# Kernel optimization log

Measured on AMD Instinct MI355X. Metric: run time of the kernel, lower is better.

Reference implementation:

```python
import jax, jax.numpy as jnp
import numpy as np

MASK_WEIGHT = 1.0
HEAD_DIM = 64
SCALING = HEAD_DIM ** -0.5


def _rotate_half(x):
    x1, x2 = jnp.split(x, 2, axis=-1)
    return jnp.concatenate([-x2, x1], axis=-1)


def _rope_tables(seq_len, dim, dtype):
    inv_freq = 1.0 / (10000.0 ** (jnp.arange(0, dim, 2, dtype=jnp.float32) / dim))
    t = jnp.arange(seq_len, dtype=jnp.float32)
    freqs = jnp.outer(t, inv_freq)                      # (s, d/2)
    cos = jnp.tile(jnp.cos(freqs), (1, 2)).astype(dtype)  # (s, d)  '(2 d)' tiling
    sin = jnp.tile(jnp.sin(freqs), (1, 2)).astype(dtype)
    return cos, sin


def _apply_rope(x, cos, sin):
    # x: (b, h, s, d); cos/sin: (s, d) broadcast over b, h
    return x * cos + _rotate_half(x) * sin


def setup_inputs() -> dict:
    key = jax.random.key(0)
    ks = jax.random.split(key, 6)
    b, h, s, d = 2, 16, 2048, 64
    d_model = h * d
    return {
        "q": jax.random.normal(ks[0], (b, h, s, d), jnp.float32),
        "k": jax.random.normal(ks[1], (b, h, s, d), jnp.float32),
        "v": jax.random.normal(ks[2], (b, h, s, d), jnp.float32),
        "attention_mask": jax.random.normal(ks[3], (1, h, s, s), jnp.float32) * 0.05,
        "out_w": jax.random.normal(ks[4], (d_model, d_model), jnp.float32) * (d_model ** -0.5),
        "out_b": jax.random.normal(ks[5], (d_model,), jnp.float32) * 0.02,
    }


def reference(q, k, v, attention_mask, out_w, out_b):
    b, h, s, d = q.shape
    cos, sin = _rope_tables(s, d, q.dtype)
    qr = _apply_rope(q, cos, sin)
    kr = _apply_rope(k, cos, sin)
    # learned per-head affinity transform of the queries: q' = (mask_weight * W) @ q
    W = attention_mask[0] * MASK_WEIGHT                    # (h, s, s), shared over batch
    qt = jnp.einsum('hqk,bhkd->bhqd', W, qr)
    # flash-style online softmax over keys == plain stable softmax (same math)
    scores = jnp.einsum('bhqd,bhkd->bhqk', qt, kr) * SCALING
    attn = jax.nn.softmax(scores, axis=-1)
    ctx = jnp.einsum('bhqk,bhkd->bhqd', attn, v)
    ctx = ctx.transpose(0, 2, 1, 3).reshape(b, s, h * d)   # (b, s, d_model)
    return ctx @ out_w.T + out_b
```

## Files before the change

### kernel.cpp

```cpp
#include <hip/hip_runtime.h>
#include <hip/hip_bf16.h>
#include <math.h>

typedef __bf16 bf16_t;
typedef __bf16 bf16x4 __attribute__((ext_vector_type(4)));
typedef __bf16 bf16x8 __attribute__((ext_vector_type(8)));
typedef float f32x4 __attribute__((ext_vector_type(4)));

#define NB 2
#define NH 16
#define SEQ 2048
#define HD 64
#define DMODEL 1024
#define QK_SCALE 0.125f
#define LOG2E 1.44269504088896340f
#define INV_2PI 0.15915494309189535f

__device__ __forceinline__ bf16_t to_bf16(float x) { return (bf16_t)x; }
#define MFMA16 __builtin_amdgcn_mfma_f32_16x16x32_bf16

__global__ __launch_bounds__(256) void k1_rope_pack(
    const float* __restrict__ q, const float* __restrict__ k, const float* __restrict__ v,
    bf16_t* __restrict__ qrT, bf16_t* __restrict__ krN, bf16_t* __restrict__ vT)
{
  __shared__ bf16_t tile[64][65];
  const int tid = threadIdx.x;
  const int blk = blockIdx.x;
  const int st = blk & 31;
  const int bh = blk >> 5;
  const int s0 = st * 64;

  const size_t base_sd = ((size_t)bh * SEQ + s0) * HD;
  const float* qb = q + base_sd;
  const float* kb = k + base_sd;
  const float* vb = v + base_sd;
  bf16_t* qrTb = qrT + (size_t)bh * HD * SEQ;
  bf16_t* krNb = krN + base_sd;
  bf16_t* vTb  = vT  + (size_t)bh * HD * SEQ;

  #pragma unroll
  for (int pp = 0; pp < 8; ++pp) {
    int idx = pp * 256 + tid;
    int sr = idx >> 5;
    int j  = idx & 31;
    float freq = __builtin_amdgcn_exp2f(-(float)j * (13.287712379549449f / 32.0f));
    float ang = (float)(s0 + sr) * freq;
    float rev = ang * INV_2PI;
    rev = rev - floorf(rev);
    float c  = __builtin_amdgcn_cosf(rev);
    float sn = __builtin_amdgcn_sinf(rev);
    float q1 = qb[sr*HD + j], q2 = qb[sr*HD + j + 32];
    tile[sr][j]      = to_bf16((q1*c - q2*sn) * QK_SCALE);
    tile[sr][j + 32] = to_bf16((q2*c + q1*sn) * QK_SCALE);
    float ka = kb[sr*HD + j], kbv = kb[sr*HD + j + 32];
    krNb[sr*HD + j]      = to_bf16(ka*c - kbv*sn);
    krNb[sr*HD + j + 32] = to_bf16(kbv*c + ka*sn);
  }
  __syncthreads();
  #pragma unroll
  for (int c = 0; c < 2; ++c) {
    int id = c*256 + tid;
    int d = id >> 3;
    int sc = (id & 7) * 8;
    bf16x8 vec;
    #pragma unroll
    for (int i = 0; i < 8; ++i) vec[i] = tile[sc + i][d];
    *(bf16x8*)&qrTb[(size_t)d * SEQ + s0 + sc] = vec;
  }
  __syncthreads();
  #pragma unroll
  for (int c = 0; c < 4; ++c) {
    int id = c*256 + tid;
    int sr = id >> 4;
    int c4 = (id & 15) * 4;
    float4 v4 = *(const float4*)&vb[sr*HD + c4];
    tile[sr][c4+0] = to_bf16(v4.x);
    tile[sr][c4+1] = to_bf16(v4.y);
    tile[sr][c4+2] = to_bf16(v4.z);
    tile[sr][c4+3] = to_bf16(v4.w);
  }
  __syncthreads();
  #pragma unroll
  for (int c = 0; c < 2; ++c) {
    int id = c*256 + tid;
    int d = id >> 3;
    int sc = (id & 7) * 8;
    bf16x8 vec;
    #pragma unroll
    for (int i = 0; i < 8; ++i) vec[i] = tile[sc + i][d];
    *(bf16x8*)&vTb[(size_t)d * SEQ + s0 + sc] = vec;
  }
}

__global__ __launch_bounds__(256) void k2_qt_gemm(
    const float* __restrict__ Wm,
    const bf16_t* __restrict__ qrT,
    bf16_t* __restrict__ qtT)
{
  __shared__ __align__(16) bf16_t A_lds[2][64*72];
  __shared__ __align__(16) bf16_t B_lds[64*72];
  const int tid = threadIdx.x;
  const int blk = blockIdx.x;
  const int n0 = (blk & 31) * 64;
  const int h = blk >> 5;
  const int wave = tid >> 6, lane = tid & 63;
  const int l15 = lane & 15, quad = lane >> 4;
  const int rs = tid >> 2, cs = (tid & 3) * 16;

  const float* Wh = Wm + (size_t)h * SEQ * SEQ + (size_t)n0 * SEQ;
  const bf16_t* A0 = qrT + ((size_t)h * HD + rs) * SEQ;
  const bf16_t* A1 = qrT + (((size_t)NH + h) * HD + rs) * SEQ;

  f32x4 acc[2][4] = {};
  float4 wreg[4];
  bf16x8 areg[2][2];

  #pragma unroll
  for (int i = 0; i < 4; ++i) wreg[i] = *(const float4*)&Wh[(size_t)rs*SEQ + cs + i*4];
  #pragma unroll
  for (int i = 0; i < 2; ++i) {
    areg[0][i] = *(const bf16x8*)&A0[cs + i*8];
    areg[1][i] = *(const bf16x8*)&A1[cs + i*8];
  }

  for (int it = 0; it < SEQ/64; ++it) {
    if (it) __syncthreads();
    #pragma unroll
    for (int i = 0; i < 2; ++i) {
      *(bf16x8*)&A_lds[0][rs*72 + cs + i*8] = areg[0][i];
      *(bf16x8*)&A_lds[1][rs*72 + cs + i*8] = areg[1][i];
      bf16x8 wb;
      float4 wa = wreg[i*2], wc = wreg[i*2+1];
      wb[0]=to_bf16(wa.x); wb[1]=to_bf16(wa.y); wb[2]=to_bf16(wa.z); wb[3]=to_bf16(wa.w);
      wb[4]=to_bf16(wc.x); wb[5]=to_bf16(wc.y); wb[6]=to_bf16(wc.z); wb[7]=to_bf16(wc.w);
      *(bf16x8*)&B_lds[rs*72 + cs + i*8] = wb;
    }
    __syncthreads();
    if (it + 1 < SEQ/64) {
      int kb = (it + 1) * 64;
      #pragma unroll
      for (int i = 0; i < 4; ++i) wreg[i] = *(const float4*)&Wh[(size_t)rs*SEQ + kb + cs + i*4];
      #pragma unroll
      for (int i = 0; i < 2; ++i) {
        areg[0][i] = *(const bf16x8*)&A0[kb + cs + i*8];
        areg[1][i] = *(const bf16x8*)&A1[kb + cs + i*8];
      }
    }
    #pragma unroll
    for (int kc = 0; kc < 2; ++kc) {
      const int off = kc*32 + quad*8;
      bf16x8 bfr[4];
      #pragma unroll
      for (int nt = 0; nt < 4; ++nt)
        bfr[nt] = *(const bf16x8*)&B_lds[(nt*16 + l15)*72 + off];
      #pragma unroll
      for (int b2 = 0; b2 < 2; ++b2) {
        bf16x8 af = *(const bf16x8*)&A_lds[b2][(wave*16 + l15)*72 + off];
        #pragma unroll
        for (int nt = 0; nt < 4; ++nt)
          acc[b2][nt] = MFMA16(af, bfr[nt], acc[b2][nt], 0, 0, 0);
      }
    }
  }
  #pragma unroll
  for (int b2 = 0; b2 < 2; ++b2)
    #pragma unroll
    for (int nt = 0; nt < 4; ++nt)
      #pragma unroll
      for (int r = 0; r < 4; ++r) {
        int d = wave*16 + quad*4 + r;
        qtT[(((size_t)b2*NH + h)*HD + d)*SEQ + n0 + nt*16 + l15] =
            to_bf16(acc[b2][nt][r] * LOG2E);
      }
}

__global__ __launch_bounds__(256, 2) void k3_flash(
    const bf16_t* __restrict__ qtT,
    const bf16_t* __restrict__ krN,
    const bf16_t* __restrict__ vT,
    bf16_t* __restrict__ ctx)
{
  __shared__ __align__(16) bf16_t K_lds[64*72];
  __shared__ __align__(16) bf16_t V_lds[64*72];
  __shared__ __align__(16) bf16_t P_lds[4][16*72];
  const int tid = threadIdx.x;
  const int blk = blockIdx.x;
  const int qt = blk & 15;
  const int bh = blk >> 4;
  const int h = bh & 15, b = bh >> 4;
  const int wave = tid >> 6, lane = tid & 63;
  const int l15 = lane & 15, quad = lane >> 4;
  const int qw = qt*128 + wave*32;
  const int srow = tid >> 3, sch = (tid & 7) * 8;

  const bf16_t* qtb = qtT + (size_t)bh * HD * SEQ;
  const bf16_t* krb = krN + (size_t)bh * SEQ * HD;
  const bf16_t* vtb = vT  + (size_t)bh * HD * SEQ;

  bf16x8 Qf[2][2];
  #pragma unroll
  for (int g = 0; g < 2; ++g)
    #pragma unroll
    for (int c = 0; c < 2; ++c)
      #pragma unroll
      for (int j = 0; j < 8; ++j)
        Qf[g][c][j] = qtb[(size_t)(c*32 + quad*8 + j)*SEQ + qw + g*16 + l15];

  bf16x8 ones;
  #pragma unroll
  for (int j = 0; j < 8; ++j) ones[j] = to_bf16(1.0f);

  f32x4 O[2][4] = {};
  f32x4 L[2] = {};

  bf16x8 kreg[2], vreg[2];
  #pragma unroll
  for (int c = 0; c < 2; ++c) {
    int row = c*32 + srow;
    kreg[c] = *(const bf16x8*)&krb[(size_t)row*HD + sch];
    vreg[c] = *(const bf16x8*)&vtb[(size_t)row*SEQ + sch];
  }

  for (int kt = 0; kt < 32; ++kt) {
    if (kt) __syncthreads();
    #pragma unroll
    for (int c = 0; c < 2; ++c) {
      int row = c*32 + srow;
      *(bf16x8*)&K_lds[row*72 + sch] = kreg[c];
      *(bf16x8*)&V_lds[row*72 + sch] = vreg[c];
    }
    __syncthreads();
    if (kt + 1 < 32) {
      #pragma unroll
      for (int c = 0; c < 2; ++c) {
        int row = c*32 + srow;
        kreg[c] = *(const bf16x8*)&krb[(size_t)((kt+1)*64 + row)*HD + sch];
        vreg[c] = *(const bf16x8*)&vtb[(size_t)row*SEQ + (kt+1)*64 + sch];
      }
    }

    bf16x8 ak[4][2], bv[4][2];
    #pragma unroll
    for (int nt = 0; nt < 4; ++nt) {
      ak[nt][0] = *(const bf16x8*)&K_lds[(nt*16 + l15)*72 + quad*8];
      ak[nt][1] = *(const bf16x8*)&K_lds[(nt*16 + l15)*72 + 32 + quad*8];
      bv[nt][0] = *(const bf16x8*)&V_lds[(nt*16 + l15)*72 + quad*8];
      bv[nt][1] = *(const bf16x8*)&V_lds[(nt*16 + l15)*72 + 32 + quad*8];
    }

    #pragma unroll
    for (int g = 0; g < 2; ++g) {
      f32x4 s[4] = {};
      #pragma unroll
      for (int nt = 0; nt < 4; ++nt) {
        s[nt] = MFMA16(ak[nt][0], Qf[g][0], s[nt], 0, 0, 0);
        s[nt] = MFMA16(ak[nt][1], Qf[g][1], s[nt], 0, 0, 0);
      }
      #pragma unroll
      for (int nt = 0; nt < 4; ++nt) {
        bf16x4 pk;
        #pragma unroll
        for (int r = 0; r < 4; ++r)
          pk[r] = to_bf16(__builtin_amdgcn_exp2f(s[nt][r]));
        *(bf16x4*)&P_lds[wave][l15*72 + nt*16 + quad*4] = pk;
      }
      bf16x8 ap0 = *(const bf16x8*)&P_lds[wave][l15*72 + quad*8];
      bf16x8 ap1 = *(const bf16x8*)&P_lds[wave][l15*72 + 32 + quad*8];
      #pragma unroll
      for (int nt = 0; nt < 4; ++nt) {
        O[g][nt] = MFMA16(ap0, bv[nt][0], O[g][nt], 0, 0, 0);
        O[g][nt] = MFMA16(ap1, bv[nt][1], O[g][nt], 0, 0, 0);
      }
      L[g] = MFMA16(ap0, ones, L[g], 0, 0, 0);
      L[g] = MFMA16(ap1, ones, L[g], 0, 0, 0);
    }
  }

  #pragma unroll
  for (int g = 0; g < 2; ++g)
    #pragma unroll
    for (int nt = 0; nt < 4; ++nt)
      #pragma unroll
      for (int r = 0; r < 4; ++r) {
        int qrow = qw + g*16 + quad*4 + r;
        float o = O[g][nt][r] / L[g][r];
        ctx[((size_t)b*SEQ + qrow)*DMODEL + h*HD + nt*16 + l15] = to_bf16(o);
      }
}

__global__ __launch_bounds__(256) void k4_proj(
    const bf16_t* __restrict__ ctx,
    const float* __restrict__ w,
    const float* __restrict__ bias,
    float* __restrict__ out)
{
  __shared__ __align__(16) bf16_t A_lds[128*72];
  __shared__ __align__(16) bf16_t B_lds[64*72];
  const int tid = threadIdx.x;
  const int blk = blockIdx.x;
  const int n0 = (blk & 15) * 64;
  const int m0 = (blk >> 4) * 128;
  const int wave = tid >> 6, lane = tid & 63;
  const int l15 = lane & 15, quad = lane >> 4;
  const int ra = tid >> 1, ca = (tid & 1) * 32;
  const int rs = tid >> 2, cs = (tid & 3) * 16;

  f32x4 acc[2][4] = {};
  bf16x8 areg[4];
  float4 wreg[4];

  #pragma unroll
  for (int i = 0; i < 4; ++i) {
    areg[i] = *(const bf16x8*)&ctx[(size_t)(m0 + ra)*DMODEL + ca + i*8];
    wreg[i] = *(const float4*)&w[(size_t)(n0 + rs)*DMODEL + cs + i*4];
  }

  for (int it = 0; it < DMODEL/64; ++it) {
    if (it) __syncthreads();
    #pragma unroll
    for (int i = 0; i < 4; ++i)
      *(bf16x8*)&A_lds[ra*72 + ca + i*8] = areg[i];
    #pragma unroll
    for (int i = 0; i < 2; ++i) {
      bf16x8 wb;
      float4 wa = wreg[i*2], wc = wreg[i*2+1];
      wb[0]=to_bf16(wa.x); wb[1]=to_bf16(wa.y); wb[2]=to_bf16(wa.z); wb[3]=to_bf16(wa.w);
      wb[4]=to_bf16(wc.x); wb[5]=to_bf16(wc.y); wb[6]=to_bf16(wc.z); wb[7]=to_bf16(wc.w);
      *(bf16x8*)&B_lds[rs*72 + cs + i*8] = wb;
    }
    __syncthreads();
    if (it + 1 < DMODEL/64) {
      int kb = (it + 1) * 64;
      #pragma unroll
      for (int i = 0; i < 4; ++i) {
        areg[i] = *(const bf16x8*)&ctx[(size_t)(m0 + ra)*DMODEL + kb + ca + i*8];
        wreg[i] = *(const float4*)&w[(size_t)(n0 + rs)*DMODEL + kb + cs + i*4];
      }
    }
    #pragma unroll
    for (int kc = 0; kc < 2; ++kc) {
      const int off = kc*32 + quad*8;
      bf16x8 bfr[4];
      #pragma unroll
      for (int nt = 0; nt < 4; ++nt)
        bfr[nt] = *(const bf16x8*)&B_lds[(nt*16 + l15)*72 + off];
      #pragma unroll
      for (int g = 0; g < 2; ++g) {
        bf16x8 af = *(const bf16x8*)&A_lds[(wave*32 + g*16 + l15)*72 + off];
        #pragma unroll
        for (int nt = 0; nt < 4; ++nt)
          acc[g][nt] = MFMA16(af, bfr[nt], acc[g][nt], 0, 0, 0);
      }
    }
  }
  #pragma unroll
  for (int nt = 0; nt < 4; ++nt) {
    float bb = bias[n0 + nt*16 + l15];
    #pragma unroll
    for (int g = 0; g < 2; ++g)
      #pragma unroll
      for (int r = 0; r < 4; ++r)
        out[(size_t)(m0 + wave*32 + g*16 + quad*4 + r)*DMODEL + n0 + nt*16 + l15] =
            acc[g][nt][r] + bb;
  }
}

extern "C" void kernel_launch(void* const* d_in, const int* in_sizes, int n_in,
                              void* d_out, int out_size, void* d_ws, size_t ws_size,
                              hipStream_t stream)
{
  const float* q     = (const float*)d_in[0];
  const float* k     = (const float*)d_in[1];
  const float* v     = (const float*)d_in[2];
  const float* mask  = (const float*)d_in[3];
  const float* out_w = (const float*)d_in[4];
  const float* out_b = (const float*)d_in[5];
  float* out = (float*)d_out;

  const size_t elems = (size_t)NB * NH * SEQ * HD;
  bf16_t* qrT = (bf16_t*)d_ws;
  bf16_t* krN = qrT + elems;
  bf16_t* vT  = krN + elems;
  bf16_t* qtT = vT  + elems;
  bf16_t* ctx = qtT + elems;

  k1_rope_pack<<<dim3(NB*NH*(SEQ/64)), dim3(256), 0, stream>>>(q, k, v, qrT, krN, vT);
  k2_qt_gemm <<<dim3(NH*(SEQ/64)),     dim3(256), 0, stream>>>(mask, qrT, qtT);
  k3_flash   <<<dim3(NB*NH*(SEQ/128)), dim3(256), 0, stream>>>(qtT, krN, vT, ctx);
  k4_proj    <<<dim3((NB*SEQ/128)*(DMODEL/64)), dim3(256), 0, stream>>>(ctx, out_w, out_b, out);
}
```

Baseline: 487.3 us.

## Use async global-to-LDS copies with double buffering and split-K flash attention

The Q-transform GEMM now uses smaller 32-column tiles (doubling the grid), double-buffered W and A tiles, and direct global-to-LDS async copies of A into an XOR-swizzled layout. The flash kernel now stages K/V with async copies into double-buffered swizzled LDS. Its four waves split the work as two query halves by two key halves, with the key-half partial O and L merged through LDS at the end. The aim is to overlap global loads with MFMA work, cut register staging and bank conflicts, and raise parallelism. The cost is more LDS per block, which may limit occupancy, plus an extra reduction step.

```diff
diff --git a/kernel.cpp b/kernel.cpp
--- a/kernel.cpp
+++ b/kernel.cpp
@@ -18,6 +18,12 @@
 
 __device__ __forceinline__ bf16_t to_bf16(float x) { return (bf16_t)x; }
 #define MFMA16 __builtin_amdgcn_mfma_f32_16x16x32_bf16
+
+__device__ __forceinline__ void async_copy16(const bf16_t* g, bf16_t* l) {
+  typedef const unsigned int __attribute__((address_space(1)))* gp_t;
+  typedef unsigned int __attribute__((address_space(3)))* lp_t;
+  __builtin_amdgcn_global_load_lds((gp_t)g, (lp_t)l, 16, 0, 0);
+}
 
 __global__ __launch_bounds__(256) void k1_rope_pack(
     const float* __restrict__ q, const float* __restrict__ k, const float* __restrict__ v,
@@ -97,81 +103,92 @@
     const bf16_t* __restrict__ qrT,
     bf16_t* __restrict__ qtT)
 {
-  __shared__ __align__(16) bf16_t A_lds[2][64*72];
-  __shared__ __align__(16) bf16_t B_lds[64*72];
+  __shared__ __align__(16) bf16_t A_lds[2][2][4096];
+  __shared__ __align__(16) bf16_t W_lds[2][32*68];
   const int tid = threadIdx.x;
   const int blk = blockIdx.x;
-  const int n0 = (blk & 31) * 64;
-  const int h = blk >> 5;
+  const int n0 = (blk & 63) * 32;
+  const int h = blk >> 6;
   const int wave = tid >> 6, lane = tid & 63;
   const int l15 = lane & 15, quad = lane >> 4;
-  const int rs = tid >> 2, cs = (tid & 3) * 16;
+  const int rs = tid >> 3, cs = (tid & 7) * 8;
+  const int b2w = wave >> 1, jbase = (wave & 1) * 4;
 
   const float* Wh = Wm + (size_t)h * SEQ * SEQ + (size_t)n0 * SEQ;
-  const bf16_t* A0 = qrT + ((size_t)h * HD + rs) * SEQ;
-  const bf16_t* A1 = qrT + (((size_t)NH + h) * HD + rs) * SEQ;
-
-  f32x4 acc[2][4] = {};
-  float4 wreg[4];
-  bf16x8 areg[2][2];
-
-  #pragma unroll
-  for (int i = 0; i < 4; ++i) wreg[i] = *(const float4*)&Wh[(size_t)rs*SEQ + cs + i*4];
-  #pragma unroll
-  for (int i = 0; i < 2; ++i) {
-    areg[0][i] = *(const bf16x8*)&A0[cs + i*8];
-    areg[1][i] = *(const bf16x8*)&A1[cs + i*8];
-  }
-
-  for (int it = 0; it < SEQ/64; ++it) {
-    if (it) __syncthreads();
-    #pragma unroll
-    for (int i = 0; i < 2; ++i) {
-      *(bf16x8*)&A_lds[0][rs*72 + cs + i*8] = areg[0][i];
-      *(bf16x8*)&A_lds[1][rs*72 + cs + i*8] = areg[1][i];
-      bf16x8 wb;
-      float4 wa = wreg[i*2], wc = wreg[i*2+1];
-      wb[0]=to_bf16(wa.x); wb[1]=to_bf16(wa.y); wb[2]=to_bf16(wa.z); wb[3]=to_bf16(wa.w);
-      wb[4]=to_bf16(wc.x); wb[5]=to_bf16(wc.y); wb[6]=to_bf16(wc.z); wb[7]=to_bf16(wc.w);
-      *(bf16x8*)&B_lds[rs*72 + cs + i*8] = wb;
-    }
+  const bf16_t* Abase = qrT + (((size_t)b2w * NH + h) * HD) * SEQ;
+
+  float4 wreg[2][2];
+
+  #define STAGE_A(kb, bufIdx)                                                  \
+    {                                                                          \
+      _Pragma("unroll")                                                        \
+      for (int j2 = 0; j2 < 4; ++j2) {                                         \
+        int j = jbase + j2;                                                    \
+        int r = j*8 + (lane >> 3);                                             \
+        int sc = (lane & 7) ^ (r & 7);                                         \
+        async_copy16(Abase + (size_t)r*SEQ + (kb) + sc*8,                      \
+                     &A_lds[bufIdx][b2w][j*512]);                              \
+      }                                                                        \
+    }
+  #define LOAD_W(kb, setIdx)                                                   \
+    {                                                                          \
+      wreg[setIdx][0] = *(const float4*)&Wh[(size_t)rs*SEQ + (kb) + cs];       \
+      wreg[setIdx][1] = *(const float4*)&Wh[(size_t)rs*SEQ + (kb) + cs + 4];   \
+    }
+  #define STORE_W(setIdx, bufIdx)                                              \
+    {                                                                          \
+      bf16x8 wb;                                                               \
+      float4 wa = wreg[setIdx][0], wc = wreg[setIdx][1];                       \
+      wb[0]=to_bf16(wa.x); wb[1]=to_bf16(wa.y); wb[2]=to_bf16(wa.z);           \
+      wb[3]=to_bf16(wa.w); wb[4]=to_bf16(wc.x); wb[5]=to_bf16(wc.y);           \
+      wb[6]=to_bf16(wc.z); wb[7]=to_bf16(wc.w);                                \
+      *(bf16x8*)&W_lds[bufIdx][rs*68 + cs] = wb;                               \
+    }
+
+  LOAD_W(0, 0);
+  STAGE_A(0, 0);
+  STORE_W(0, 0);
+  LOAD_W(64, 1);
+  __syncthreads();
+
+  f32x4 acc[2][2] = {};
+
+  for (int it = 0; it < 32; ++it) {
+    const int buf = it & 1;
+    if (it + 2 < 32) LOAD_W((it+2)*64, it & 1);
+    if (it + 1 < 32) STAGE_A((it+1)*64, buf ^ 1);
+    #pragma unroll
+    for (int kc = 0; kc < 2; ++kc) {
+      bf16x8 bfr[2];
+      #pragma unroll
+      for (int nt = 0; nt < 2; ++nt)
+        bfr[nt] = *(const bf16x8*)&W_lds[buf][(nt*16 + l15)*68 + kc*32 + quad*8];
+      #pragma unroll
+      for (int b2 = 0; b2 < 2; ++b2) {
+        int r = wave*16 + l15;
+        bf16x8 af = *(const bf16x8*)&A_lds[buf][b2][r*64 + (((kc*4+quad) ^ (l15&7))*8)];
+        #pragma unroll
+        for (int nt = 0; nt < 2; ++nt)
+          acc[b2][nt] = MFMA16(af, bfr[nt], acc[b2][nt], 0, 0, 0);
+      }
+    }
+    if (it + 1 < 32) STORE_W((it+1) & 1, buf ^ 1);
     __syncthreads();
-    if (it + 1 < SEQ/64) {
-      int kb = (it + 1) * 64;
-      #pragma unroll
-      for (int i = 0; i < 4; ++i) wreg[i] = *(const float4*)&Wh[(size_t)rs*SEQ + kb + cs + i*4];
-      #pragma unroll
-      for (int i = 0; i < 2; ++i) {
-        areg[0][i] = *(const bf16x8*)&A0[kb + cs + i*8];
-        areg[1][i] = *(const bf16x8*)&A1[kb + cs + i*8];
-      }
-    }
-    #pragma unroll
-    for (int kc = 0; kc < 2; ++kc) {
-      const int off = kc*32 + quad*8;
-      bf16x8 bfr[4];
-      #pragma unroll
-      for (int nt = 0; nt < 4; ++nt)
-        bfr[nt] = *(const bf16x8*)&B_lds[(nt*16 + l15)*72 + off];
-      #pragma unroll
-      for (int b2 = 0; b2 < 2; ++b2) {
-        bf16x8 af = *(const bf16x8*)&A_lds[b2][(wave*16 + l15)*72 + off];
-        #pragma unroll
-        for (int nt = 0; nt < 4; ++nt)
-          acc[b2][nt] = MFMA16(af, bfr[nt], acc[b2][nt], 0, 0, 0);
-      }
-    }
-  }
+  }
+
   #pragma unroll
   for (int b2 = 0; b2 < 2; ++b2)
     #pragma unroll
-    for (int nt = 0; nt < 4; ++nt)
+    for (int nt = 0; nt < 2; ++nt)
       #pragma unroll
       for (int r = 0; r < 4; ++r) {
         int d = wave*16 + quad*4 + r;
         qtT[(((size_t)b2*NH + h)*HD + d)*SEQ + n0 + nt*16 + l15] =
             to_bf16(acc[b2][nt][r] * LOG2E);
       }
+  #undef STAGE_A
+  #undef LOAD_W
+  #undef STORE_W
 }
 
 __global__ __launch_bounds__(256, 2) void k3_flash(
@@ -180,18 +197,17 @@
     const bf16_t* __restrict__ vT,
     bf16_t* __restrict__ ctx)
 {
-  __shared__ __align__(16) bf16_t K_lds[64*72];
-  __shared__ __align__(16) bf16_t V_lds[64*72];
+  __shared__ __align__(16) bf16_t KV_lds[2][4][4096];
   __shared__ __align__(16) bf16_t P_lds[4][16*72];
   const int tid = threadIdx.x;
   const int blk = blockIdx.x;
-  const int qt = blk & 15;
-  const int bh = blk >> 4;
+  const int qt = blk & 31;
+  const int bh = blk >> 5;
   const int h = bh & 15, b = bh >> 4;
   const int wave = tid >> 6, lane = tid & 63;
   const int l15 = lane & 15, quad = lane >> 4;
-  const int qw = qt*128 + wave*32;
-  const int srow = tid >> 3, sch = (tid & 7) * 8;
+  const int qhalf = wave & 1, khalf = wave >> 1;
+  const int qw = qt*64 + qhalf*32;
 
   const bf16_t* qtb = qtT + (size_t)bh * HD * SEQ;
   const bf16_t* krb = krN + (size_t)bh * SEQ * HD;
@@ -213,40 +229,39 @@
   f32x4 O[2][4] = {};
   f32x4 L[2] = {};
 
-  bf16x8 kreg[2], vreg[2];
-  #pragma unroll
-  for (int c = 0; c < 2; ++c) {
-    int row = c*32 + srow;
-    kreg[c] = *(const bf16x8*)&krb[(size_t)row*HD + sch];
-    vreg[c] = *(const bf16x8*)&vtb[(size_t)row*SEQ + sch];
-  }
-
-  for (int kt = 0; kt < 32; ++kt) {
-    if (kt) __syncthreads();
-    #pragma unroll
-    for (int c = 0; c < 2; ++c) {
-      int row = c*32 + srow;
-      *(bf16x8*)&K_lds[row*72 + sch] = kreg[c];
-      *(bf16x8*)&V_lds[row*72 + sch] = vreg[c];
-    }
-    __syncthreads();
-    if (kt + 1 < 32) {
-      #pragma unroll
-      for (int c = 0; c < 2; ++c) {
-        int row = c*32 + srow;
-        kreg[c] = *(const bf16x8*)&krb[(size_t)((kt+1)*64 + row)*HD + sch];
-        vreg[c] = *(const bf16x8*)&vtb[(size_t)row*SEQ + (kt+1)*64 + sch];
-      }
-    }
-
+  #define STAGE_KV(kt, bufIdx)                                                 \
+    {                                                                          \
+      const int k0 = (kt)*64;                                                  \
+      bf16_t* dbase = &KV_lds[bufIdx][wave][0];                                \
+      _Pragma("unroll")                                                        \
+      for (int j = 0; j < 8; ++j) {                                            \
+        int r = j*8 + (lane >> 3);                                             \
+        int sc = (lane & 7) ^ (r & 7);                                         \
+        const bf16_t* src;                                                     \
+        if (wave < 2) src = krb + (size_t)(wave*1024 + k0 + r)*HD + sc*8;      \
+        else          src = vtb + (size_t)r*SEQ + (wave-2)*1024 + k0 + sc*8;   \
+        async_copy16(src, dbase + j*512);                                      \
+      }                                                                        \
+    }
+
+  STAGE_KV(0, 0);
+  __syncthreads();
+
+  for (int kt = 0; kt < 16; ++kt) {
+    const int buf = kt & 1;
+    if (kt + 1 < 16) STAGE_KV(kt + 1, buf ^ 1);
+
+    const bf16_t* Kt = &KV_lds[buf][khalf][0];
+    const bf16_t* Vt = &KV_lds[buf][2 + khalf][0];
     bf16x8 ak[4][2], bv[4][2];
     #pragma unroll
-    for (int nt = 0; nt < 4; ++nt) {
-      ak[nt][0] = *(const bf16x8*)&K_lds[(nt*16 + l15)*72 + quad*8];
-      ak[nt][1] = *(const bf16x8*)&K_lds[(nt*16 + l15)*72 + 32 + quad*8];
-      bv[nt][0] = *(const bf16x8*)&V_lds[(nt*16 + l15)*72 + quad*8];
-      bv[nt][1] = *(const bf16x8*)&V_lds[(nt*16 + l15)*72 + 32 + quad*8];
-    }
+    for (int nt = 0; nt < 4; ++nt)
+      #pragma unroll
+      for (int hh = 0; hh < 2; ++hh) {
+        int idx = (nt*16 + l15)*64 + (((hh*4 + quad) ^ (l15 & 7))*8);
+        ak[nt][hh] = *(const bf16x8*)&Kt[idx];
+        bv[nt][hh] = *(const bf16x8*)&Vt[idx];
+      }
 
     #pragma unroll
     for (int g = 0; g < 2; ++g) {
@@ -274,18 +289,47 @@
       L[g] = MFMA16(ap0, ones, L[g], 0, 0, 0);
       L[g] = MFMA16(ap1, ones, L[g], 0, 0, 0);
     }
-  }
-
-  #pragma unroll
-  for (int g = 0; g < 2; ++g)
-    #pragma unroll
-    for (int nt = 0; nt < 4; ++nt)
-      #pragma unroll
-      for (int r = 0; r < 4; ++r) {
-        int qrow = qw + g*16 + quad*4 + r;
-        float o = O[g][nt][r] / L[g][r];
-        ctx[((size_t)b*SEQ + qrow)*DMODEL + h*HD + nt*16 + l15] = to_bf16(o);
-      }
+    __syncthreads();
+  }
+  #undef STAGE_KV
+
+  float* Os = (float*)&KV_lds[0][0][0];
+  float* Ls = Os + 4096;
+  if (khalf == 1) {
+    int base = (qhalf*64 + lane)*32;
+    #pragma unroll
+    for (int g = 0; g < 2; ++g)
+      #pragma unroll
+      for (int nt = 0; nt < 4; ++nt)
+        #pragma unroll
+        for (int r = 0; r < 4; ++r)
+          Os[base + g*16 + nt*4 + r] = O[g][nt][r];
+    int lb = (qhalf*64 + lane)*8;
+    #pragma unroll
+    for (int g = 0; g < 2; ++g)
+      #pragma unroll
+      for (int r = 0; r < 4; ++r)
+        Ls[lb + g*4 + r] = L[g][r];
+  }
+  __syncthreads();
+  if (khalf == 0) {
+    int base = (qhalf*64 + lane)*32;
+    int lb = (qhalf*64 + lane)*8;
+    #pragma unroll
+    for (int g = 0; g < 2; ++g) {
+      float lsum[4];
+      #pragma unroll
+      for (int r = 0; r < 4; ++r) lsum[r] = L[g][r] + Ls[lb + g*4 + r];
+      #pragma unroll
+      for (int nt = 0; nt < 4; ++nt)
+        #pragma unroll
+        for (int r = 0; r < 4; ++r) {
+          float o = (O[g][nt][r] + Os[base + g*16 + nt*4 + r]) / lsum[r];
+          int qrow = qw + g*16 + quad*4 + r;
+          ctx[((size_t)b*SEQ + qrow)*DMODEL + h*HD + nt*16 + l15] = to_bf16(o);
+        }
+    }
+  }
 }
 
 __global__ __launch_bounds__(256) void k4_proj(
@@ -385,7 +429,7 @@
   bf16_t* ctx = qtT + elems;
 
   k1_rope_pack<<<dim3(NB*NH*(SEQ/64)), dim3(256), 0, stream>>>(q, k, v, qrT, krN, vT);
-  k2_qt_gemm <<<dim3(NH*(SEQ/64)),     dim3(256), 0, stream>>>(mask, qrT, qtT);
-  k3_flash   <<<dim3(NB*NH*(SEQ/128)), dim3(256), 0, stream>>>(qtT, krN, vT, ctx);
+  k2_qt_gemm <<<dim3(NH*(SEQ/32)),     dim3(256), 0, stream>>>(mask, qrT, qtT);
+  k3_flash   <<<dim3(NB*NH*(SEQ/64)),  dim3(256), 0, stream>>>(qtT, krN, vT, ctx);
   k4_proj    <<<dim3((NB*SEQ/128)*(DMODEL/64)), dim3(256), 0, stream>>>(ctx, out_w, out_b, out);
 }
```

Result: slower. 524.3 us (+7.6%).
